# Optimization experiments

Hardware: AMD Instinct MI355X
Metric: run time of the kernel (lower is better)

Reference implementation:

```python
import jax, jax.numpy as jnp
import numpy as np

B, IN_DIM, D, P = 256, 1024, 512, 2048


def setup_inputs() -> dict:
    key = jax.random.key(0)
    ks = jax.random.split(key, 7)
    return {
        "x": jax.random.normal(ks[0], (B, IN_DIM), dtype=jnp.float32),
        "y": jax.random.randint(ks[1], (B,), 0, P),
        "Wb": jax.random.normal(ks[2], (D, IN_DIM), dtype=jnp.float32) * 0.02,
        "bb": jax.random.normal(ks[3], (D,), dtype=jnp.float32) * 0.02,
        "Wm": jax.random.normal(ks[4], (P, D), dtype=jnp.float32) * 0.02,
        "bm": jax.random.normal(ks[5], (P,), dtype=jnp.float32) * 0.02,
        "proxies": jax.random.normal(ks[6], (P, D), dtype=jnp.float32),
    }


def reference(x, y, Wb, bb, Wm, bm, proxies):
    # backbone: Linear(in_dim -> D)
    feat = x @ Wb.T + bb                         # [B, D]
    # L2-norm regularizer: mean of per-row L2 norms
    reg_e = jnp.mean(jnp.sqrt(jnp.sum(feat * feat, axis=1)))
    # multi: classification head Linear(D -> P)
    out = feat @ Wm.T + bm                       # [B, P]
    # squared euclidean distance to each proxy (broadcast diff + square + sum)
    den = jnp.sum((feat[:, None, :] - proxies[None, :, :]) ** 2, axis=2)  # [B, P]
    # cross-entropy on negated distances
    logp = jax.nn.log_softmax(-den, axis=1)      # [B, P]
    loss = -jnp.mean(jnp.take_along_axis(logp, y[:, None], axis=1))
    return out, loss, reg_e
```

## Files before the change

kernel.cpp:

```cpp
#include <hip/hip_runtime.h>
#include <hip/hip_bf16.h>
#include <math.h>

#define NB   256
#define KIN  1024
#define ND   512
#define NP   2048
#define NTOT 4096

typedef __bf16 bf16x8 __attribute__((ext_vector_type(8)));
typedef float  f32x4  __attribute__((ext_vector_type(4)));
typedef unsigned short ush8 __attribute__((ext_vector_type(8)));

#define OFF_WPB    0u
#define OFF_FEAT32 4194304u
#define OFF_FEATB  4718592u
#define OFF_PN2    4980736u
#define OFF_LOGITS 4988928u

__device__ __forceinline__ ush8 pack8(float4 f0, float4 f1) {
    union { ush8 v; __hip_bfloat162 h[4]; } o;
    o.h[0] = __float22bfloat162_rn(make_float2(f0.x, f0.y));
    o.h[1] = __float22bfloat162_rn(make_float2(f0.z, f0.w));
    o.h[2] = __float22bfloat162_rn(make_float2(f1.x, f1.y));
    o.h[3] = __float22bfloat162_rn(make_float2(f1.z, f1.w));
    return o.v;
}
__device__ __forceinline__ unsigned short f2bf(float v) {
    union { __hip_bfloat16 h; unsigned short u; } c;
    c.h = __float2bfloat16(v);
    return c.u;
}
__device__ __forceinline__ bf16x8 ldf8(const float* p) {
    float4 v0 = *(const float4*)p, v1 = *(const float4*)(p + 4);
    union { ush8 u; bf16x8 b; } c;
    c.u = pack8(v0, v1);
    return c.b;
}

__global__ __launch_bounds__(256) void k1_featprep(
    const float* __restrict__ x, const float* __restrict__ Wb,
    const float* __restrict__ bb,
    const float* __restrict__ Wm, const float* __restrict__ prox,
    unsigned short* __restrict__ WPb, float* __restrict__ pn2,
    float* __restrict__ feat32, unsigned short* __restrict__ featb,
    float* __restrict__ tail)
{
    __shared__ __align__(16) float smemf[4 * 1056];
    const int t = threadIdx.x, lane = t & 63, w = t >> 6;

    if (blockIdx.x >= 128) {
        const int pb = blockIdx.x - 128;
        if (pb == 0 && t < 2) tail[t] = 0.f;
#pragma unroll
        for (int i = 0; i < 4; ++i) {
            const int r = pb * 16 + w * 4 + i;
            const float* src = (r < NP) ? (Wm + (size_t)r * ND)
                                        : (prox + (size_t)(r - NP) * ND);
            float4 v0 = *(const float4*)(src + lane * 8);
            float4 v1 = *(const float4*)(src + lane * 8 + 4);
            if (r < NP) {
                *(ush8*)(WPb + (size_t)r * ND + lane * 8) = pack8(v0, v1);
            } else {
                float s = v0.x*v0.x + v0.y*v0.y + v0.z*v0.z + v0.w*v0.w
                        + v1.x*v1.x + v1.y*v1.y + v1.z*v1.z + v1.w*v1.w;
#pragma unroll
                for (int off = 32; off; off >>= 1) s += __shfl_down(s, off);
                if (lane == 0) pn2[r - NP] = s;
                float4 d0 = make_float4(v0.x + v0.x, v0.y + v0.y,
                                        v0.z + v0.z, v0.w + v0.w);
                float4 d1 = make_float4(v1.x + v1.x, v1.y + v1.y,
                                        v1.z + v1.z, v1.w + v1.w);
                *(ush8*)(WPb + (size_t)r * ND + lane * 8) = pack8(d0, d1);
            }
        }
        return;
    }

    const int m0 = (blockIdx.x >> 4) * 32, n0 = (blockIdx.x & 15) * 32;
    const int fr = lane & 15, ck = (lane >> 4) * 8;
    const float* pA0 = x  + (size_t)(m0 + fr) * KIN + w * 256 + ck;
    const float* pA1 = pA0 + 16 * KIN;
    const float* pB0 = Wb + (size_t)(n0 + fr) * KIN + w * 256 + ck;
    const float* pB1 = pB0 + 16 * KIN;
    f32x4 acc[2][2] = {};
#pragma unroll
    for (int ks = 0; ks < 8; ++ks) {
        const int off = ks * 32;
        bf16x8 af0 = ldf8(pA0 + off);
        bf16x8 af1 = ldf8(pA1 + off);
        bf16x8 bf0 = ldf8(pB0 + off);
        bf16x8 bf1 = ldf8(pB1 + off);
        acc[0][0] = __builtin_amdgcn_mfma_f32_16x16x32_bf16(af0, bf0, acc[0][0], 0, 0, 0);
        acc[0][1] = __builtin_amdgcn_mfma_f32_16x16x32_bf16(af0, bf1, acc[0][1], 0, 0, 0);
        acc[1][0] = __builtin_amdgcn_mfma_f32_16x16x32_bf16(af1, bf0, acc[1][0], 0, 0, 0);
        acc[1][1] = __builtin_amdgcn_mfma_f32_16x16x32_bf16(af1, bf1, acc[1][1], 0, 0, 0);
    }
    float* red = smemf + w * 1056;
    const int q = lane >> 4;
#pragma unroll
    for (int i = 0; i < 2; ++i)
#pragma unroll
        for (int j = 0; j < 2; ++j)
#pragma unroll
            for (int r = 0; r < 4; ++r)
                red[(16 * i + q * 4 + r) * 33 + 16 * j + fr] = acc[i][j][r];
    __syncthreads();
#pragma unroll
    for (int e = t; e < 1024; e += 256) {
        const int row = e >> 5, col = e & 31;
        const int idx = row * 33 + col;
        float v = smemf[idx] + smemf[idx + 1056]
                + smemf[idx + 2112] + smemf[idx + 3168];
        const int n = n0 + col;
        const float val = v + bb[n];
        feat32[(m0 + row) * ND + n] = val;
        featb [(m0 + row) * ND + n] = f2bf(val);
    }
}

__global__ __launch_bounds__(256) void k2_head(
    const unsigned short* __restrict__ featb,
    const unsigned short* __restrict__ WPb,
    const float* __restrict__ bm, const float* __restrict__ pn2,
    float* __restrict__ out, float* __restrict__ logits)
{
    __shared__ unsigned short As[2][64 * 32];
    __shared__ unsigned short Bs[2][64 * 32];
    const int t = threadIdx.x, lane = t & 63, w = t >> 6;
    const int n0 = blockIdx.x * 64;
    const int m0 = blockIdx.y * 64;
    const int srow = t >> 2, sc = (t & 3) * 8;
    const unsigned short* gA = featb + (size_t)(m0 + srow) * ND + sc;
    const unsigned short* gB = WPb   + (size_t)(n0 + srow) * ND + sc;
    ush8 va = *(const ush8*)gA;
    ush8 vb = *(const ush8*)gB;
    f32x4 acc[2][2] = {};
    const int wm = (w >> 1) * 32, wn = (w & 1) * 32;
    const int fr = lane & 15, fcol = (lane >> 4) * 8;

    for (int ks = 0; ks < ND / 32; ++ks) {
        *(ush8*)&As[ks & 1][srow * 32 + sc] = va;
        *(ush8*)&Bs[ks & 1][srow * 32 + sc] = vb;
        __syncthreads();
        if (ks + 1 < ND / 32) {
            va = *(const ush8*)(gA + (ks + 1) * 32);
            vb = *(const ush8*)(gB + (ks + 1) * 32);
        }
        const unsigned short* as = &As[ks & 1][0];
        const unsigned short* bs = &Bs[ks & 1][0];
        bf16x8 af0 = *(const bf16x8*)&as[(wm      + fr) * 32 + fcol];
        bf16x8 af1 = *(const bf16x8*)&as[(wm + 16 + fr) * 32 + fcol];
        bf16x8 bf0 = *(const bf16x8*)&bs[(wn      + fr) * 32 + fcol];
        bf16x8 bf1 = *(const bf16x8*)&bs[(wn + 16 + fr) * 32 + fcol];
        acc[0][0] = __builtin_amdgcn_mfma_f32_16x16x32_bf16(af0, bf0, acc[0][0], 0, 0, 0);
        acc[0][1] = __builtin_amdgcn_mfma_f32_16x16x32_bf16(af0, bf1, acc[0][1], 0, 0, 0);
        acc[1][0] = __builtin_amdgcn_mfma_f32_16x16x32_bf16(af1, bf0, acc[1][0], 0, 0, 0);
        acc[1][1] = __builtin_amdgcn_mfma_f32_16x16x32_bf16(af1, bf1, acc[1][1], 0, 0, 0);
    }

    const bool isProxy = (n0 >= NP);
    const int q = lane >> 4;
#pragma unroll
    for (int i = 0; i < 2; ++i)
#pragma unroll
        for (int j = 0; j < 2; ++j) {
            const int n = n0 + wn + 16 * j + fr;
            const float cadd = isProxy ? pn2[n - NP] : bm[n];
#pragma unroll
            for (int r = 0; r < 4; ++r) {
                const int m = m0 + wm + 16 * i + q * 4 + r;
                const float v = acc[i][j][r];
                if (isProxy) logits[m * NP + (n - NP)] = v - cadd;
                else         out[m * NP + n] = v + cadd;
            }
        }
}

__device__ __forceinline__ float block_reduce(float v, float* sred, int op)
{
    const int lane = threadIdx.x & 63, wave = threadIdx.x >> 6;
#pragma unroll
    for (int off = 32; off; off >>= 1) {
        float o = __shfl_down(v, off);
        v = op ? fmaxf(v, o) : (v + o);
    }
    if (lane == 0) sred[wave] = v;
    __syncthreads();
    if (threadIdx.x == 0) {
        float r = sred[0];
#pragma unroll
        for (int wv = 1; wv < 4; ++wv) r = op ? fmaxf(r, sred[wv]) : (r + sred[wv]);
        sred[0] = r;
    }
    __syncthreads();
    float r = sred[0];
    __syncthreads();
    return r;
}

__global__ __launch_bounds__(256) void k3_loss(
    const float* __restrict__ feat32, const float* __restrict__ logits,
    const int* __restrict__ y, float* __restrict__ tail)
{
    __shared__ float sred[4];
    const int b = blockIdx.x, t = threadIdx.x;

    float v0 = feat32[b * ND + t];
    float v1 = feat32[b * ND + t + 256];
    float fn2 = block_reduce(v0 * v0 + v1 * v1, sred, 0);

    const float* lr = logits + (size_t)b * NP;
    float lv[8], mx = -INFINITY;
#pragma unroll
    for (int j = 0; j < 8; ++j) { lv[j] = lr[t + 256 * j]; mx = fmaxf(mx, lv[j]); }
    float MX = block_reduce(mx, sred, 1);
    float es = 0.f;
#pragma unroll
    for (int j = 0; j < 8; ++j) es += __expf(lv[j] - MX);
    float SUM = block_reduce(es, sred, 0);

    if (t == 0) {
        float ly = lr[y[b]];
        float lp = ly - MX - __logf(SUM);
        atomicAdd(&tail[0], -lp * (1.0f / (float)NB));
        atomicAdd(&tail[1], sqrtf(fn2) * (1.0f / (float)NB));
    }
}

extern "C" void kernel_launch(void* const* d_in, const int* in_sizes, int n_in,
                              void* d_out, int out_size, void* d_ws, size_t ws_size,
                              hipStream_t stream)
{
    const float* x       = (const float*)d_in[0];
    const int*   y       = (const int*)  d_in[1];
    const float* Wb      = (const float*)d_in[2];
    const float* bb      = (const float*)d_in[3];
    const float* Wm      = (const float*)d_in[4];
    const float* bm      = (const float*)d_in[5];
    const float* proxies = (const float*)d_in[6];

    char* ws = (char*)d_ws;
    unsigned short* WPb    = (unsigned short*)(ws + OFF_WPB);
    float*          feat32 = (float*)(ws + OFF_FEAT32);
    unsigned short* featb  = (unsigned short*)(ws + OFF_FEATB);
    float*          pn2    = (float*)(ws + OFF_PN2);
    float*          logits = (float*)(ws + OFF_LOGITS);

    float* out  = (float*)d_out;
    float* tail = out + (size_t)NB * NP;

    k1_featprep<<<dim3(384), dim3(256), 0, stream>>>(
        x, Wb, bb, Wm, proxies, WPb, pn2, feat32, featb, tail);
    k2_head<<<dim3(NTOT / 64, NB / 64), dim3(256), 0, stream>>>(
        featb, WPb, bm, pn2, out, logits);
    k3_loss<<<dim3(NB), dim3(256), 0, stream>>>(feat32, logits, y, tail);
}
```

Before: 99.72 us.

## Fuse loss kernel into head GEMM epilogue via partial softmax and last-block reduction

Removes the separate loss kernel. Each proxy tile of the head GEMM now computes per-row partial max and sum-exp over its 64 logits and writes them to workspace. An atomic counter per row-block picks the last-arriving block, which merges the partials, computes the feature norms and the target log-prob, and accumulates the final scalars. This saves one launch and a full reread of the logits, but adds fences, atomics and serial tail work in the last block of each row-block.

```diff
diff --git a/kernel.cpp b/kernel.cpp
--- a/kernel.cpp
+++ b/kernel.cpp
@@ -17,6 +17,9 @@
 #define OFF_FEATB  4718592u
 #define OFF_PN2    4980736u
 #define OFF_LOGITS 4988928u
+#define OFF_PMX    7086080u
+#define OFF_PSUM   7118848u
+#define OFF_CNT    7151616u
 
 __device__ __forceinline__ ush8 pack8(float4 f0, float4 f1) {
     union { ush8 v; __hip_bfloat162 h[4]; } o;
@@ -44,14 +47,17 @@
     const float* __restrict__ Wm, const float* __restrict__ prox,
     unsigned short* __restrict__ WPb, float* __restrict__ pn2,
     float* __restrict__ feat32, unsigned short* __restrict__ featb,
-    float* __restrict__ tail)
+    float* __restrict__ tail, int* __restrict__ cnt)
 {
     __shared__ __align__(16) float smemf[4 * 1056];
     const int t = threadIdx.x, lane = t & 63, w = t >> 6;
 
     if (blockIdx.x >= 128) {
         const int pb = blockIdx.x - 128;
-        if (pb == 0 && t < 2) tail[t] = 0.f;
+        if (pb == 0) {
+            if (t < 2) tail[t] = 0.f;
+            if (t < 4) cnt[t] = 0;
+        }
 #pragma unroll
         for (int i = 0; i < 4; ++i) {
             const int r = pb * 16 + w * 4 + i;
@@ -119,14 +125,37 @@
     }
 }
 
+__device__ __forceinline__ float block_reduce_sum(float v, float* sred)
+{
+    const int lane = threadIdx.x & 63, wave = threadIdx.x >> 6;
+#pragma unroll
+    for (int off = 32; off; off >>= 1) v += __shfl_down(v, off);
+    if (lane == 0) sred[wave] = v;
+    __syncthreads();
+    float r = 0.f;
+    if (threadIdx.x == 0) {
+        r = sred[0] + sred[1] + sred[2] + sred[3];
+    }
+    __syncthreads();
+    return r;
+}
+
 __global__ __launch_bounds__(256) void k2_head(
     const unsigned short* __restrict__ featb,
     const unsigned short* __restrict__ WPb,
     const float* __restrict__ bm, const float* __restrict__ pn2,
-    float* __restrict__ out, float* __restrict__ logits)
+    const float* __restrict__ feat32, const int* __restrict__ y,
+    float* __restrict__ out, float* __restrict__ logits,
+    float* __restrict__ pmx, float* __restrict__ psum,
+    int* __restrict__ cnt, float* __restrict__ tail)
 {
-    __shared__ unsigned short As[2][64 * 32];
-    __shared__ unsigned short Bs[2][64 * 32];
+    __shared__ __align__(16) char smem[16896];
+    __shared__ float sred[4];
+    __shared__ int slast;
+    unsigned short (*As)[64 * 32] = (unsigned short (*)[64 * 32])smem;
+    unsigned short (*Bs)[64 * 32] = (unsigned short (*)[64 * 32])(smem + 8192);
+    float* tile = (float*)smem;
+
     const int t = threadIdx.x, lane = t & 63, w = t >> 6;
     const int n0 = blockIdx.x * 64;
     const int m0 = blockIdx.y * 64;
@@ -161,70 +190,107 @@
 
     const bool isProxy = (n0 >= NP);
     const int q = lane >> 4;
+
+    if (!isProxy) {
+#pragma unroll
+        for (int i = 0; i < 2; ++i)
+#pragma unroll
+            for (int j = 0; j < 2; ++j) {
+                const int n = n0 + wn + 16 * j + fr;
+                const float cadd = bm[n];
+#pragma unroll
+                for (int r = 0; r < 4; ++r) {
+                    const int m = m0 + wm + 16 * i + q * 4 + r;
+                    out[m * NP + n] = acc[i][j][r] + cadd;
+                }
+            }
+        return;
+    }
+
+    __syncthreads();
 #pragma unroll
     for (int i = 0; i < 2; ++i)
 #pragma unroll
         for (int j = 0; j < 2; ++j) {
-            const int n = n0 + wn + 16 * j + fr;
-            const float cadd = isProxy ? pn2[n - NP] : bm[n];
+            const int ln = wn + 16 * j + fr;
+            const int n  = n0 + ln;
+            const float cadd = pn2[n - NP];
 #pragma unroll
             for (int r = 0; r < 4; ++r) {
-                const int m = m0 + wm + 16 * i + q * 4 + r;
-                const float v = acc[i][j][r];
-                if (isProxy) logits[m * NP + (n - NP)] = v - cadd;
-                else         out[m * NP + n] = v + cadd;
+                const int lm = wm + 16 * i + q * 4 + r;
+                const float v = acc[i][j][r] - cadd;
+                logits[(m0 + lm) * NP + (n - NP)] = v;
+                tile[lm * 66 + ln] = v;
             }
         }
-}
-
-__device__ __forceinline__ float block_reduce(float v, float* sred, int op)
-{
-    const int lane = threadIdx.x & 63, wave = threadIdx.x >> 6;
-#pragma unroll
-    for (int off = 32; off; off >>= 1) {
-        float o = __shfl_down(v, off);
-        v = op ? fmaxf(v, o) : (v + o);
-    }
-    if (lane == 0) sred[wave] = v;
-    __syncthreads();
-    if (threadIdx.x == 0) {
-        float r = sred[0];
-#pragma unroll
-        for (int wv = 1; wv < 4; ++wv) r = op ? fmaxf(r, sred[wv]) : (r + sred[wv]);
-        sred[0] = r;
-    }
-    __syncthreads();
-    float r = sred[0];
-    __syncthreads();
-    return r;
-}
-
-__global__ __launch_bounds__(256) void k3_loss(
-    const float* __restrict__ feat32, const float* __restrict__ logits,
-    const int* __restrict__ y, float* __restrict__ tail)
-{
-    __shared__ float sred[4];
-    const int b = blockIdx.x, t = threadIdx.x;
-
-    float v0 = feat32[b * ND + t];
-    float v1 = feat32[b * ND + t + 256];
-    float fn2 = block_reduce(v0 * v0 + v1 * v1, sred, 0);
-
-    const float* lr = logits + (size_t)b * NP;
-    float lv[8], mx = -INFINITY;
-#pragma unroll
-    for (int j = 0; j < 8; ++j) { lv[j] = lr[t + 256 * j]; mx = fmaxf(mx, lv[j]); }
-    float MX = block_reduce(mx, sred, 1);
-    float es = 0.f;
-#pragma unroll
-    for (int j = 0; j < 8; ++j) es += __expf(lv[j] - MX);
-    float SUM = block_reduce(es, sred, 0);
-
+    __syncthreads();
+
+    {
+        const int row = t >> 2, g = t & 3;
+        const float* tr = tile + row * 66 + g * 16;
+        float mx = -INFINITY;
+        float vv[16];
+#pragma unroll
+        for (int k = 0; k < 16; ++k) { vv[k] = tr[k]; mx = fmaxf(mx, vv[k]); }
+        float m1 = fmaxf(mx, __shfl_xor(mx, 1));
+        float MT = fmaxf(m1, __shfl_xor(m1, 2));
+        float s = 0.f;
+#pragma unroll
+        for (int k = 0; k < 16; ++k) s += __expf(vv[k] - MT);
+        s += __shfl_xor(s, 1);
+        s += __shfl_xor(s, 2);
+        if (g == 0) {
+            const int pt = blockIdx.x - 32;
+            pmx [pt * 256 + m0 + row] = MT;
+            psum[pt * 256 + m0 + row] = s;
+        }
+    }
+    __syncthreads();
     if (t == 0) {
-        float ly = lr[y[b]];
-        float lp = ly - MX - __logf(SUM);
-        atomicAdd(&tail[0], -lp * (1.0f / (float)NB));
-        atomicAdd(&tail[1], sqrtf(fn2) * (1.0f / (float)NB));
+        __threadfence();
+        const int old = atomicAdd(&cnt[blockIdx.y], 1);
+        slast = (old == 31);
+    }
+    __syncthreads();
+    if (!slast) return;
+
+    __threadfence();
+    const int row = t >> 2, g = t & 3, grow = m0 + row;
+
+    float mx = -INFINITY;
+#pragma unroll
+    for (int p = g * 8; p < g * 8 + 8; ++p) mx = fmaxf(mx, pmx[p * 256 + grow]);
+    float m1 = fmaxf(mx, __shfl_xor(mx, 1));
+    float MX = fmaxf(m1, __shfl_xor(m1, 2));
+    float s = 0.f;
+#pragma unroll
+    for (int p = g * 8; p < g * 8 + 8; ++p)
+        s += psum[p * 256 + grow] * __expf(pmx[p * 256 + grow] - MX);
+    s += __shfl_xor(s, 1);
+    s += __shfl_xor(s, 2);
+
+    float n2 = 0.f;
+    const float4* fp = (const float4*)(feat32 + (size_t)grow * ND + g * 128);
+#pragma unroll
+    for (int k = 0; k < 32; ++k) {
+        float4 v = fp[k];
+        n2 += v.x * v.x + v.y * v.y + v.z * v.z + v.w * v.w;
+    }
+    n2 += __shfl_xor(n2, 1);
+    n2 += __shfl_xor(n2, 2);
+
+    float lpv = 0.f, nmv = 0.f;
+    if (g == 0) {
+        const float ly = logits[(size_t)grow * NP + y[grow]];
+        lpv = ly - MX - __logf(s);
+        nmv = sqrtf(n2);
+    }
+    float S1 = block_reduce_sum(lpv, sred);
+    __syncthreads();
+    float S2 = block_reduce_sum(nmv, sred);
+    if (t == 0) {
+        atomicAdd(&tail[0], -S1 * (1.0f / (float)NB));
+        atomicAdd(&tail[1],  S2 * (1.0f / (float)NB));
     }
 }
 
@@ -246,13 +312,15 @@
     unsigned short* featb  = (unsigned short*)(ws + OFF_FEATB);
     float*          pn2    = (float*)(ws + OFF_PN2);
     float*          logits = (float*)(ws + OFF_LOGITS);
+    float*          pmx    = (float*)(ws + OFF_PMX);
+    float*          psum   = (float*)(ws + OFF_PSUM);
+    int*            cnt    = (int*)  (ws + OFF_CNT);
 
     float* out  = (float*)d_out;
     float* tail = out + (size_t)NB * NP;
 
     k1_featprep<<<dim3(384), dim3(256), 0, stream>>>(
-        x, Wb, bb, Wm, proxies, WPb, pn2, feat32, featb, tail);
+        x, Wb, bb, Wm, proxies, WPb, pn2, feat32, featb, tail, cnt);
     k2_head<<<dim3(NTOT / 64, NB / 64), dim3(256), 0, stream>>>(
-        featb, WPb, bm, pn2, out, logits);
-    k3_loss<<<dim3(NB), dim3(256), 0, stream>>>(feat32, logits, y, tail);
-}
+        featb, WPb, bm, pn2, feat32, y, out, logits, pmx, psum, cnt, tail);
+}
```

Measured after the change: 99.85 us. Within noise of the previous version (+0.1%).
